# Kernel optimization log

Hardware: AMD Instinct MI355X
Metric: run time of the kernel (lower is better)

The kernel has to match this reference:

```python
import jax, jax.numpy as jnp
import numpy as np

ALPHA = 0.5
EPS = 1e-6


def setup_inputs() -> dict:
    key = jax.random.key(0)
    k1, k2, k3 = jax.random.split(key, 3)
    B, N = 8192, 4096
    y_pred = jax.random.uniform(k1, (B, N), dtype=jnp.float32)
    y_true = jax.random.randint(k2, (B, N), 0, 2).astype(jnp.float32)
    depth_weights = jax.random.uniform(k3, (B, N), dtype=jnp.float32)
    return {"y_pred": y_pred, "y_true": y_true, "depth_weights": depth_weights}


def reference(y_pred, y_true, depth_weights):
    B, N = y_true.shape
    # --- weighted BCE ---
    bce = -(y_true * jnp.log(y_pred + EPS) + (1.0 - y_true) * jnp.log(1.0 - y_pred + EPS))
    wbce = jnp.mean(depth_weights * bce)

    # --- continuity-weighted loss: max run of correct predictions per row ---
    y_bin = (y_pred > 0.5).astype(y_true.dtype)
    correct = (y_bin == y_true)  # bool [B, N]
    idx = jnp.arange(N, dtype=jnp.int32)
    # position (1-based) of most recent incorrect element; 0 if none yet
    reset = jnp.where(correct, 0, idx + 1)  # [B, N]
    last_reset = jax.lax.cummax(reset, axis=1)  # [B, N]
    streak = (idx + 1)[None, :] - last_reset  # current run length at each position
    max_streak = jnp.max(streak, axis=1).astype(jnp.float32)  # [B]
    cwl = jnp.mean(1.0 - max_streak / N)

    return ALPHA * wbce + (1.0 - ALPHA) * cwl
```

## Files before the change

### kernel.cpp

```cpp
#include <hip/hip_runtime.h>

#define EPS 1e-6f

struct RunStats { int len, pre, suf, mx; };

__device__ inline RunStats rcombine(const RunStats& a, const RunStats& b) {
    RunStats r;
    r.len = a.len + b.len;
    r.pre = (a.pre == a.len) ? (a.len + b.pre) : a.pre;
    r.suf = (b.suf == b.len) ? (b.len + a.suf) : b.suf;
    r.mx  = max(max(a.mx, b.mx), a.suf + b.pre);
    return r;
}

__global__ __launch_bounds__(256) void row_kernel(
        const float* __restrict__ yp, const float* __restrict__ yt,
        const float* __restrict__ dw,
        float* __restrict__ row_wbce, int* __restrict__ row_streak) {
    const int row  = blockIdx.x;
    const int lane = threadIdx.x & 63;
    const int wave = threadIdx.x >> 6;
    const long base = (long)row * 4096 + wave * 1024 + lane * 16;

    float4 p[4], t[4], w[4];
    #pragma unroll
    for (int q = 0; q < 4; ++q) {
        p[q] = *(const float4*)(yp + base + q * 4);
        t[q] = *(const float4*)(yt + base + q * 4);
        w[q] = *(const float4*)(dw + base + q * 4);
    }

    float sum = 0.0f;
    unsigned mask = 0;
    #pragma unroll
    for (int q = 0; q < 4; ++q) {
        const float pp[4] = {p[q].x, p[q].y, p[q].z, p[q].w};
        const float tt[4] = {t[q].x, t[q].y, t[q].z, t[q].w};
        const float ww[4] = {w[q].x, w[q].y, w[q].z, w[q].w};
        #pragma unroll
        for (int c = 0; c < 4; ++c) {
            const bool tb = tt[c] != 0.0f;
            const float v = (tb ? pp[c] : 1.0f - pp[c]) + EPS;
            sum = fmaf(ww[c], __logf(v), sum);
            const bool pb = pp[c] > 0.5f;
            mask |= (unsigned)(pb == tb) << (q * 4 + c);
        }
    }

    int pre = __builtin_ctz(~mask);
    int suf = __builtin_clz(~(mask << 16));
    int mx = 0;
    { unsigned x = mask; while (x) { x &= (x << 1); ++mx; } }

    #pragma unroll
    for (int off = 32; off; off >>= 1) sum += __shfl_down(sum, off);

    int packed = pre | (suf << 10) | (mx << 20);
    int alen = 16;
    #pragma unroll
    for (int off = 1; off < 32; off <<= 1) {
        const int o = __shfl_down(packed, off);
        const int apre = packed & 1023, asuf = (packed >> 10) & 1023, amx = packed >> 20;
        const int bpre = o & 1023,      bsuf = (o >> 10) & 1023,      bmx = o >> 20;
        const int npre = (apre == alen) ? (alen + bpre) : apre;
        const int nsuf = (bsuf == alen) ? (alen + asuf) : bsuf;
        const int nmx  = max(max(amx, bmx), asuf + bpre);
        packed = npre | (nsuf << 10) | (nmx << 20);
        alen <<= 1;
    }
    RunStats g;
    {
        const int o = __shfl_down(packed, 32);
        const int apre = packed & 1023, asuf = (packed >> 10) & 1023, amx = packed >> 20;
        const int bpre = o & 1023,      bsuf = (o >> 10) & 1023,      bmx = o >> 20;
        g.len = 1024;
        g.pre = (apre == 512) ? (512 + bpre) : apre;
        g.suf = (bsuf == 512) ? (512 + asuf) : bsuf;
        g.mx  = max(max(amx, bmx), asuf + bpre);
    }

    __shared__ RunStats sstat[4];
    __shared__ float ssum[4];
    if (lane == 0) { sstat[wave] = g; ssum[wave] = sum; }
    __syncthreads();
    if (threadIdx.x == 0) {
        RunStats r = rcombine(rcombine(sstat[0], sstat[1]), rcombine(sstat[2], sstat[3]));
        row_wbce[row]   = -(ssum[0] + ssum[1] + ssum[2] + ssum[3]);
        row_streak[row] = r.mx;
    }
}

__global__ __launch_bounds__(1024) void finalize_kernel(
        const float* __restrict__ row_wbce, const int* __restrict__ row_streak,
        int rows, float* __restrict__ out) {
    double s = 0.0;
    long long st = 0;
    for (int i = threadIdx.x; i < rows; i += 1024) {
        s  += (double)row_wbce[i];
        st += (long long)row_streak[i];
    }
    __shared__ double sd[1024];
    __shared__ long long sl[1024];
    sd[threadIdx.x] = s; sl[threadIdx.x] = st;
    __syncthreads();
    for (int o = 512; o; o >>= 1) {
        if (threadIdx.x < o) {
            sd[threadIdx.x] += sd[threadIdx.x + o];
            sl[threadIdx.x] += sl[threadIdx.x + o];
        }
        __syncthreads();
    }
    if (threadIdx.x == 0) {
        const double total = (double)rows * 4096.0;
        const double wbce = sd[0] / total;
        const double cwl  = 1.0 - (double)sl[0] / total;
        out[0] = (float)(0.5 * wbce + 0.5 * cwl);
    }
}

extern "C" void kernel_launch(void* const* d_in, const int* in_sizes, int n_in,
                              void* d_out, int out_size, void* d_ws, size_t ws_size,
                              hipStream_t stream) {
    const float* yp = (const float*)d_in[0];
    const float* yt = (const float*)d_in[1];
    const float* dw = (const float*)d_in[2];
    float* out = (float*)d_out;

    const int rows = in_sizes[0] / 4096;
    float* row_wbce   = (float*)d_ws;
    int*   row_streak = (int*)((char*)d_ws + (size_t)rows * sizeof(float));

    row_kernel<<<rows, 256, 0, stream>>>(yp, yt, dw, row_wbce, row_streak);
    finalize_kernel<<<1, 1024, 0, stream>>>(row_wbce, row_streak, rows, out);
}
```

Baseline: 349.4 us.

## Coalesce loads and compute run stats from wave ballot masks

Each lane now reads strided float4 chunks (lane*4, stride 64 float4s) so every load instruction is fully coalesced across the wave. Correctness bits go into 64-bit wave-wide ballots, and each wave computes prefix, suffix and max run directly from the 16 ballot words. This replaces the per-lane bitmask and the packed shuffle-combine tree. It also switches to log2 with a single ln2 rescale at the end. The max-run loop iterates once per unit of streak length on uniform 64-bit values, which could be slow when runs are long, but random inputs keep runs short.

```diff
diff --git a/kernel.cpp b/kernel.cpp
--- a/kernel.cpp
+++ b/kernel.cpp
@@ -1,6 +1,7 @@
 #include <hip/hip_runtime.h>
 
 #define EPS 1e-6f
+#define LN2F 0.69314718055994530942f
 
 struct RunStats { int len, pre, suf, mx; };
 
@@ -20,72 +21,99 @@
     const int row  = blockIdx.x;
     const int lane = threadIdx.x & 63;
     const int wave = threadIdx.x >> 6;
-    const long base = (long)row * 4096 + wave * 1024 + lane * 16;
+    const long base = (long)row * 4096 + wave * 1024 + lane * 4;
 
-    float4 p[4], t[4], w[4];
+    const float4* pp = (const float4*)(yp + base);
+    const float4* tp = (const float4*)(yt + base);
+    const float4* wp = (const float4*)(dw + base);
+
+    float4 P[4], T[4], W[4];
     #pragma unroll
     for (int q = 0; q < 4; ++q) {
-        p[q] = *(const float4*)(yp + base + q * 4);
-        t[q] = *(const float4*)(yt + base + q * 4);
-        w[q] = *(const float4*)(dw + base + q * 4);
+        P[q] = pp[q * 64];
+        T[q] = tp[q * 64];
+        W[q] = wp[q * 64];
     }
 
     float sum = 0.0f;
-    unsigned mask = 0;
+    unsigned long long m[4][4];
     #pragma unroll
     for (int q = 0; q < 4; ++q) {
-        const float pp[4] = {p[q].x, p[q].y, p[q].z, p[q].w};
-        const float tt[4] = {t[q].x, t[q].y, t[q].z, t[q].w};
-        const float ww[4] = {w[q].x, w[q].y, w[q].z, w[q].w};
+        const float pv[4] = {P[q].x, P[q].y, P[q].z, P[q].w};
+        const float tv[4] = {T[q].x, T[q].y, T[q].z, T[q].w};
+        const float wv[4] = {W[q].x, W[q].y, W[q].z, W[q].w};
         #pragma unroll
         for (int c = 0; c < 4; ++c) {
-            const bool tb = tt[c] != 0.0f;
-            const float v = (tb ? pp[c] : 1.0f - pp[c]) + EPS;
-            sum = fmaf(ww[c], __logf(v), sum);
-            const bool pb = pp[c] > 0.5f;
-            mask |= (unsigned)(pb == tb) << (q * 4 + c);
+            const bool tb = tv[c] != 0.0f;
+            const float sel = tb ? pv[c] : 1.0f - pv[c];
+            sum = fmaf(wv[c], __log2f(sel + EPS), sum);
+            const bool correct = (pv[c] > 0.5f) == tb;
+            m[q][c] = __ballot(correct);
         }
     }
 
-    int pre = __builtin_ctz(~mask);
-    int suf = __builtin_clz(~(mask << 16));
+    int pre;
+    {
+        int j = 0;
+        while (j < 4 && (m[j][0] & m[j][1] & m[j][2] & m[j][3]) == ~0ULL) ++j;
+        if (j == 4) pre = 1024;
+        else {
+            int best = 1 << 30;
+            for (int c = 0; c < 4; ++c) {
+                unsigned long long z = ~m[j][c];
+                if (z) best = min(best, 4 * (int)__builtin_ctzll(z) + c);
+            }
+            pre = j * 256 + best;
+        }
+    }
+    int suf;
+    {
+        int j = 3;
+        while (j >= 0 && (m[j][0] & m[j][1] & m[j][2] & m[j][3]) == ~0ULL) --j;
+        if (j < 0) suf = 1024;
+        else {
+            int last = -1;
+            for (int c = 0; c < 4; ++c) {
+                unsigned long long z = ~m[j][c];
+                if (z) last = max(last, 4 * (63 - (int)__builtin_clzll(z)) + c);
+            }
+            suf = (3 - j) * 256 + (255 - last);
+        }
+    }
     int mx = 0;
-    { unsigned x = mask; while (x) { x &= (x << 1); ++mx; } }
+    {
+        unsigned long long x[4][4];
+        unsigned long long any = 0;
+        for (int j = 0; j < 4; ++j)
+            for (int c = 0; c < 4; ++c) { x[j][c] = m[j][c]; any |= m[j][c]; }
+        while (any) {
+            ++mx;
+            any = 0;
+            for (int j = 3; j >= 0; --j) {
+                const unsigned long long n0 =
+                    (x[j][3] << 1) | (j ? (x[j - 1][3] >> 63) : 0ULL);
+                x[j][3] &= x[j][2];
+                x[j][2] &= x[j][1];
+                x[j][1] &= x[j][0];
+                x[j][0] &= n0;
+                any |= x[j][0] | x[j][1] | x[j][2] | x[j][3];
+            }
+        }
+    }
 
     #pragma unroll
     for (int off = 32; off; off >>= 1) sum += __shfl_down(sum, off);
 
-    int packed = pre | (suf << 10) | (mx << 20);
-    int alen = 16;
-    #pragma unroll
-    for (int off = 1; off < 32; off <<= 1) {
-        const int o = __shfl_down(packed, off);
-        const int apre = packed & 1023, asuf = (packed >> 10) & 1023, amx = packed >> 20;
-        const int bpre = o & 1023,      bsuf = (o >> 10) & 1023,      bmx = o >> 20;
-        const int npre = (apre == alen) ? (alen + bpre) : apre;
-        const int nsuf = (bsuf == alen) ? (alen + asuf) : bsuf;
-        const int nmx  = max(max(amx, bmx), asuf + bpre);
-        packed = npre | (nsuf << 10) | (nmx << 20);
-        alen <<= 1;
-    }
-    RunStats g;
-    {
-        const int o = __shfl_down(packed, 32);
-        const int apre = packed & 1023, asuf = (packed >> 10) & 1023, amx = packed >> 20;
-        const int bpre = o & 1023,      bsuf = (o >> 10) & 1023,      bmx = o >> 20;
-        g.len = 1024;
-        g.pre = (apre == 512) ? (512 + bpre) : apre;
-        g.suf = (bsuf == 512) ? (512 + asuf) : bsuf;
-        g.mx  = max(max(amx, bmx), asuf + bpre);
-    }
-
     __shared__ RunStats sstat[4];
     __shared__ float ssum[4];
-    if (lane == 0) { sstat[wave] = g; ssum[wave] = sum; }
+    if (lane == 0) {
+        RunStats g; g.len = 1024; g.pre = pre; g.suf = suf; g.mx = mx;
+        sstat[wave] = g; ssum[wave] = sum;
+    }
     __syncthreads();
     if (threadIdx.x == 0) {
         RunStats r = rcombine(rcombine(sstat[0], sstat[1]), rcombine(sstat[2], sstat[3]));
-        row_wbce[row]   = -(ssum[0] + ssum[1] + ssum[2] + ssum[3]);
+        row_wbce[row]   = -LN2F * (ssum[0] + ssum[1] + ssum[2] + ssum[3]);
         row_streak[row] = r.mx;
     }
 }
```

After: 384.0 us. 9.9% more time.

## Coalesce row loads, transpose correctness bits via LDS, use log2 and branchless max-run

Applied to the files above, without the earlier changes.

Each lane now loads four float4s strided by 64 lanes instead of sixteen contiguous floats, so wave-level accesses are fully coalesced. Because each lane no longer owns a contiguous 16-element segment, correctness bits are written to shared memory and re-gathered so each lane rebuilds a contiguous 16-bit mask for the run-length scan. The per-element log becomes log2 with a single ln2 scale at the end, and the data-dependent while loop for the longest run is replaced by a fixed doubling/binary search. The cost is an extra shared-memory exchange and a block barrier.

```diff
diff --git a/kernel.cpp b/kernel.cpp
--- a/kernel.cpp
+++ b/kernel.cpp
@@ -1,6 +1,7 @@
 #include <hip/hip_runtime.h>
 
 #define EPS 1e-6f
+#define LN2F 0.69314718055994530942f
 
 struct RunStats { int len, pre, suf, mx; };
 
@@ -20,37 +21,66 @@
     const int row  = blockIdx.x;
     const int lane = threadIdx.x & 63;
     const int wave = threadIdx.x >> 6;
-    const long base = (long)row * 4096 + wave * 1024 + lane * 16;
+    const long base = (long)row * 4096 + wave * 1024 + lane * 4;
 
-    float4 p[4], t[4], w[4];
+    const float4* pp = (const float4*)(yp + base);
+    const float4* tp = (const float4*)(yt + base);
+    const float4* wp = (const float4*)(dw + base);
+
+    float4 P[4], T[4], W[4];
     #pragma unroll
     for (int q = 0; q < 4; ++q) {
-        p[q] = *(const float4*)(yp + base + q * 4);
-        t[q] = *(const float4*)(yt + base + q * 4);
-        w[q] = *(const float4*)(dw + base + q * 4);
+        P[q] = pp[q * 64];
+        T[q] = tp[q * 64];
+        W[q] = wp[q * 64];
     }
 
     float sum = 0.0f;
-    unsigned mask = 0;
+    unsigned nibs = 0;
     #pragma unroll
     for (int q = 0; q < 4; ++q) {
-        const float pp[4] = {p[q].x, p[q].y, p[q].z, p[q].w};
-        const float tt[4] = {t[q].x, t[q].y, t[q].z, t[q].w};
-        const float ww[4] = {w[q].x, w[q].y, w[q].z, w[q].w};
+        const float pv[4] = {P[q].x, P[q].y, P[q].z, P[q].w};
+        const float tv[4] = {T[q].x, T[q].y, T[q].z, T[q].w};
+        const float wv[4] = {W[q].x, W[q].y, W[q].z, W[q].w};
         #pragma unroll
         for (int c = 0; c < 4; ++c) {
-            const bool tb = tt[c] != 0.0f;
-            const float v = (tb ? pp[c] : 1.0f - pp[c]) + EPS;
-            sum = fmaf(ww[c], __logf(v), sum);
-            const bool pb = pp[c] > 0.5f;
-            mask |= (unsigned)(pb == tb) << (q * 4 + c);
+            const bool tb = tv[c] != 0.0f;
+            const float sel = tb ? pv[c] : 1.0f - pv[c];
+            sum = fmaf(wv[c], __log2f(sel + EPS), sum);
+            const bool correct = (pv[c] > 0.5f) == tb;
+            nibs |= (unsigned)correct << (8 * q + c);
         }
     }
 
-    int pre = __builtin_ctz(~mask);
-    int suf = __builtin_clz(~(mask << 16));
-    int mx = 0;
-    { unsigned x = mask; while (x) { x &= (x << 1); ++mx; } }
+    __shared__ unsigned nibbuf[256];
+    nibbuf[wave * 64 + lane] = nibs;
+    __syncthreads();
+    const uint4 d = *(const uint4*)&nibbuf[wave * 64 + 4 * (lane & 15)];
+    const int qs = (lane >> 4) * 8;
+    const unsigned mask = ((d.x >> qs) & 0xFu)
+                        | (((d.y >> qs) & 0xFu) << 4)
+                        | (((d.z >> qs) & 0xFu) << 8)
+                        | (((d.w >> qs) & 0xFu) << 12);
+
+    const int pre = __builtin_ctz(~mask);
+    const int suf = __builtin_clz(~(mask << 16));
+    int mx;
+    {
+        const unsigned p1 = mask;
+        const unsigned p2 = p1 & (p1 << 1);
+        const unsigned p4 = p2 & (p2 << 2);
+        const unsigned p8 = p4 & (p4 << 4);
+        unsigned z; int len;
+        if (p8)      { z = p8; len = 8; }
+        else if (p4) { z = p4; len = 4; }
+        else if (p2) { z = p2; len = 2; }
+        else         { z = p1; len = 1; }
+        { const unsigned t = (z << 8) & p8; if (t) { z = t; len += 8; } }
+        { const unsigned t = (z << 4) & p4; if (t) { z = t; len += 4; } }
+        { const unsigned t = (z << 2) & p2; if (t) { z = t; len += 2; } }
+        { const unsigned t = (z << 1) & p1; if (t) { z = t; len += 1; } }
+        mx = mask ? len : 0;
+    }
 
     #pragma unroll
     for (int off = 32; off; off >>= 1) sum += __shfl_down(sum, off);
@@ -85,7 +115,7 @@
     __syncthreads();
     if (threadIdx.x == 0) {
         RunStats r = rcombine(rcombine(sstat[0], sstat[1]), rcombine(sstat[2], sstat[3]));
-        row_wbce[row]   = -(ssum[0] + ssum[1] + ssum[2] + ssum[3]);
+        row_wbce[row]   = -LN2F * (ssum[0] + ssum[1] + ssum[2] + ssum[3]);
         row_streak[row] = r.mx;
     }
 }
```

Result: no change. 348.7 us (-0.2%).

## Process one row per wavefront with coalesced chunks and ballot-based run tracking

Applied to the files above, without the earlier changes.

Each wavefront now owns a whole row and walks it in 16 coalesced 256-element chunks, using a 3-deep register prefetch ring. Correctness bits come from wave ballots, and a sequential run/max state carries across chunks, which replaces the packed shuffle scan and the shared-memory block combine. The log is computed as log2 with the ln2 scale applied once at the end. This removes the cross-wave sync and the scan overhead but adds a serial dependence across chunks and a data-dependent while loop.

```diff
diff --git a/kernel.cpp b/kernel.cpp
--- a/kernel.cpp
+++ b/kernel.cpp
@@ -1,92 +1,92 @@
 #include <hip/hip_runtime.h>
 
 #define EPS 1e-6f
-
-struct RunStats { int len, pre, suf, mx; };
-
-__device__ inline RunStats rcombine(const RunStats& a, const RunStats& b) {
-    RunStats r;
-    r.len = a.len + b.len;
-    r.pre = (a.pre == a.len) ? (a.len + b.pre) : a.pre;
-    r.suf = (b.suf == b.len) ? (b.len + a.suf) : b.suf;
-    r.mx  = max(max(a.mx, b.mx), a.suf + b.pre);
-    return r;
-}
+#define LN2F 0.69314718055994530942f
 
 __global__ __launch_bounds__(256) void row_kernel(
         const float* __restrict__ yp, const float* __restrict__ yt,
         const float* __restrict__ dw,
         float* __restrict__ row_wbce, int* __restrict__ row_streak) {
-    const int row  = blockIdx.x;
     const int lane = threadIdx.x & 63;
     const int wave = threadIdx.x >> 6;
-    const long base = (long)row * 4096 + wave * 1024 + lane * 16;
+    const int row  = blockIdx.x * 4 + wave;
+    const long base = (long)row * 4096 + lane * 4;
 
-    float4 p[4], t[4], w[4];
+    const float4* pp = (const float4*)(yp + base);
+    const float4* tp = (const float4*)(yt + base);
+    const float4* wp = (const float4*)(dw + base);
+
+    float4 P[3], T[3], W[3];
     #pragma unroll
-    for (int q = 0; q < 4; ++q) {
-        p[q] = *(const float4*)(yp + base + q * 4);
-        t[q] = *(const float4*)(yt + base + q * 4);
-        w[q] = *(const float4*)(dw + base + q * 4);
+    for (int k = 0; k < 3; ++k) {
+        P[k] = pp[k * 64];
+        T[k] = tp[k * 64];
+        W[k] = wp[k * 64];
     }
 
     float sum = 0.0f;
-    unsigned mask = 0;
+    int run = 0;
+    int mxr = 0;
+
     #pragma unroll
-    for (int q = 0; q < 4; ++q) {
-        const float pp[4] = {p[q].x, p[q].y, p[q].z, p[q].w};
-        const float tt[4] = {t[q].x, t[q].y, t[q].z, t[q].w};
-        const float ww[4] = {w[q].x, w[q].y, w[q].z, w[q].w};
+    for (int ch = 0; ch < 16; ++ch) {
+        const int s = ch % 3;
+        const float4 p = P[s], t = T[s], w = W[s];
+        if (ch + 3 < 16) {
+            P[s] = pp[(ch + 3) * 64];
+            T[s] = tp[(ch + 3) * 64];
+            W[s] = wp[(ch + 3) * 64];
+        }
+
+        const float pv[4] = {p.x, p.y, p.z, p.w};
+        const float tv[4] = {t.x, t.y, t.z, t.w};
+        const float wv[4] = {w.x, w.y, w.z, w.w};
+        unsigned long long B[4];
         #pragma unroll
         for (int c = 0; c < 4; ++c) {
-            const bool tb = tt[c] != 0.0f;
-            const float v = (tb ? pp[c] : 1.0f - pp[c]) + EPS;
-            sum = fmaf(ww[c], __logf(v), sum);
-            const bool pb = pp[c] > 0.5f;
-            mask |= (unsigned)(pb == tb) << (q * 4 + c);
+            const bool tb = tv[c] != 0.0f;
+            const float sel = tb ? pv[c] : 1.0f - pv[c];
+            sum = fmaf(wv[c], __log2f(sel + EPS), sum);
+            B[c] = __ballot((pv[c] > 0.5f) == tb);
+        }
+
+        const unsigned long long all = B[0] & B[1] & B[2] & B[3];
+        if (all == ~0ULL) {
+            run += 256;
+            mxr = max(mxr, run);
+        } else {
+            int pre = 1 << 30;
+            #pragma unroll
+            for (int c = 0; c < 4; ++c) {
+                const unsigned long long z = ~B[c];
+                if (z) pre = min(pre, 4 * (int)__builtin_ctzll(z) + c);
+            }
+            mxr = max(mxr, run + pre);
+            unsigned long long x0 = B[0], x1 = B[1], x2 = B[2], x3 = B[3];
+            int it = 0;
+            while (x0 | x1 | x2 | x3) {
+                ++it;
+                const unsigned long long t3 = x3 << 1;
+                x3 &= x2; x2 &= x1; x1 &= x0; x0 &= t3;
+            }
+            mxr = max(mxr, it);
+            int last = -1;
+            #pragma unroll
+            for (int c = 0; c < 4; ++c) {
+                const unsigned long long z = ~B[c];
+                if (z) last = max(last, 4 * (63 - (int)__builtin_clzll(z)) + c);
+            }
+            run = 255 - last;
         }
     }
-
-    int pre = __builtin_ctz(~mask);
-    int suf = __builtin_clz(~(mask << 16));
-    int mx = 0;
-    { unsigned x = mask; while (x) { x &= (x << 1); ++mx; } }
+    mxr = max(mxr, run);
 
     #pragma unroll
     for (int off = 32; off; off >>= 1) sum += __shfl_down(sum, off);
 
-    int packed = pre | (suf << 10) | (mx << 20);
-    int alen = 16;
-    #pragma unroll
-    for (int off = 1; off < 32; off <<= 1) {
-        const int o = __shfl_down(packed, off);
-        const int apre = packed & 1023, asuf = (packed >> 10) & 1023, amx = packed >> 20;
-        const int bpre = o & 1023,      bsuf = (o >> 10) & 1023,      bmx = o >> 20;
-        const int npre = (apre == alen) ? (alen + bpre) : apre;
-        const int nsuf = (bsuf == alen) ? (alen + asuf) : bsuf;
-        const int nmx  = max(max(amx, bmx), asuf + bpre);
-        packed = npre | (nsuf << 10) | (nmx << 20);
-        alen <<= 1;
-    }
-    RunStats g;
-    {
-        const int o = __shfl_down(packed, 32);
-        const int apre = packed & 1023, asuf = (packed >> 10) & 1023, amx = packed >> 20;
-        const int bpre = o & 1023,      bsuf = (o >> 10) & 1023,      bmx = o >> 20;
-        g.len = 1024;
-        g.pre = (apre == 512) ? (512 + bpre) : apre;
-        g.suf = (bsuf == 512) ? (512 + asuf) : bsuf;
-        g.mx  = max(max(amx, bmx), asuf + bpre);
-    }
-
-    __shared__ RunStats sstat[4];
-    __shared__ float ssum[4];
-    if (lane == 0) { sstat[wave] = g; ssum[wave] = sum; }
-    __syncthreads();
-    if (threadIdx.x == 0) {
-        RunStats r = rcombine(rcombine(sstat[0], sstat[1]), rcombine(sstat[2], sstat[3]));
-        row_wbce[row]   = -(ssum[0] + ssum[1] + ssum[2] + ssum[3]);
-        row_streak[row] = r.mx;
+    if (lane == 0) {
+        row_wbce[row]   = -LN2F * sum;
+        row_streak[row] = mxr;
     }
 }
 
@@ -130,6 +130,6 @@
     float* row_wbce   = (float*)d_ws;
     int*   row_streak = (int*)((char*)d_ws + (size_t)rows * sizeof(float));
 
-    row_kernel<<<rows, 256, 0, stream>>>(yp, yt, dw, row_wbce, row_streak);
+    row_kernel<<<rows / 4, 256, 0, stream>>>(yp, yt, dw, row_wbce, row_streak);
     finalize_kernel<<<1, 1024, 0, stream>>>(row_wbce, row_streak, rows, out);
 }
```

Result: no change. 353.5 us (+1.2%).
